# Optimization experiments

Measured on AMD Instinct MI355X. Metric: run time of the kernel, lower is better.

## Reference

```python
import jax, jax.numpy as jnp
import numpy as np

N = 2097152  # batch of 3x3 matrices


def setup_inputs() -> dict:
    key = jax.random.key(0)
    k1, k2 = jax.random.split(key)
    rotation = jax.random.normal(k1, (N, 3, 3), dtype=jnp.float32)
    # learned parameter: eye(3) + 1e-3 * randn, per __init__
    mat = jnp.eye(3, dtype=jnp.float32) + 0.001 * jax.random.normal(k2, (3, 3), dtype=jnp.float32)
    return {"rotation": rotation, "mat": mat}


def reference(rotation, mat):
    # new_mat = mat @ rotation (mat broadcast over batch)  -> [N,3,3]
    new_mat = jnp.einsum('ab,nbc->nac', mat, rotation)
    # polar rotation factor via batched 3x3 SVD: R = U @ V^T
    U, S, Vh = jnp.linalg.svd(new_mat, full_matrices=False)
    out = jnp.einsum('nab,nbc->nac', U, Vh)  # torch: U @ V.transpose == U @ Vh
    logdet = jnp.zeros((rotation.shape[0],), dtype=rotation.dtype)
    return out, logdet
```

## Files before the change

### kernel.cpp

```cpp
#include <hip/hip_runtime.h>
#include <math.h>


typedef float v2f __attribute__((ext_vector_type(2)));
typedef float v4f __attribute__((ext_vector_type(4)));

#define NEWTON_ITERS 6
#define NS_ITERS 2

__device__ __forceinline__ void polar_pair(
    v2f& x00, v2f& x01, v2f& x02,
    v2f& x10, v2f& x11, v2f& x12,
    v2f& x20, v2f& x21, v2f& x22)
{
    #pragma unroll
    for (int it = 0; it < NEWTON_ITERS; ++it) {
        v2f c00 = x11*x22 - x12*x21;
        v2f c01 = x12*x20 - x10*x22;
        v2f c02 = x10*x21 - x11*x20;
        v2f c10 = x02*x21 - x01*x22;
        v2f c11 = x00*x22 - x02*x20;
        v2f c12 = x01*x20 - x00*x21;
        v2f c20 = x01*x12 - x02*x11;
        v2f c21 = x02*x10 - x00*x12;
        v2f c22 = x00*x11 - x01*x10;

        v2f det = x00*c00 + x01*c01 + x02*c02;

        float d0 = det.x, d1 = det.y;
        float ad0 = fmaxf(fabsf(d0), 1e-30f);
        float ad1 = fmaxf(fabsf(d1), 1e-30f);
        float z0 = __builtin_amdgcn_exp2f(__builtin_amdgcn_logf(ad0) * (-1.0f/3.0f));
        float z1 = __builtin_amdgcn_exp2f(__builtin_amdgcn_logf(ad1) * (-1.0f/3.0f));
        v2f s = {0.5f * z0, 0.5f * z1};
        v2f u = {copysignf(0.5f * z0 * z0, d0), copysignf(0.5f * z1 * z1, d1)};

        x00 = s*x00 + u*c00;  x01 = s*x01 + u*c01;  x02 = s*x02 + u*c02;
        x10 = s*x10 + u*c10;  x11 = s*x11 + u*c11;  x12 = s*x12 + u*c12;
        x20 = s*x20 + u*c20;  x21 = s*x21 + u*c21;  x22 = s*x22 + u*c22;
    }

    #pragma unroll
    for (int it = 0; it < NS_ITERS; ++it) {
        v2f s00 = x00*x00 + x10*x10 + x20*x20;
        v2f s01 = x00*x01 + x10*x11 + x20*x21;
        v2f s02 = x00*x02 + x10*x12 + x20*x22;
        v2f s11 = x01*x01 + x11*x11 + x21*x21;
        v2f s12 = x01*x02 + x11*x12 + x21*x22;
        v2f s22 = x02*x02 + x12*x12 + x22*x22;
        v2f t00 = 1.5f - 0.5f*s00, t01 = -0.5f*s01, t02 = -0.5f*s02;
        v2f t11 = 1.5f - 0.5f*s11, t12 = -0.5f*s12;
        v2f t22 = 1.5f - 0.5f*s22;
        v2f y00 = x00*t00 + x01*t01 + x02*t02;
        v2f y01 = x00*t01 + x01*t11 + x02*t12;
        v2f y02 = x00*t02 + x01*t12 + x02*t22;
        v2f y10 = x10*t00 + x11*t01 + x12*t02;
        v2f y11 = x10*t01 + x11*t11 + x12*t12;
        v2f y12 = x10*t02 + x11*t12 + x12*t22;
        v2f y20 = x20*t00 + x21*t01 + x22*t02;
        v2f y21 = x20*t01 + x21*t11 + x22*t12;
        v2f y22 = x20*t02 + x21*t12 + x22*t22;
        x00=y00; x01=y01; x02=y02;
        x10=y10; x11=y11; x12=y12;
        x20=y20; x21=y21; x22=y22;
    }
}

__global__ __launch_bounds__(256) void polar3x3_wave_kernel(
    const float* __restrict__ rot,
    const float* __restrict__ mat,
    float* __restrict__ out,
    int n)
{
    __shared__ float lds[4608];
    const int t    = threadIdx.x;
    const int lane = t & 63;
    const int w    = t >> 6;
    const long long blockBase = (long long)blockIdx.x * 512;
    const long long waveBase  = blockBase + (long long)w * 128;
    float* wlds = lds + w * 1152;

    const float m00 = mat[0], m01 = mat[1], m02 = mat[2];
    const float m10 = mat[3], m11 = mat[4], m12 = mat[5];
    const float m20 = mat[6], m21 = mat[7], m22 = mat[8];

    const bool full = (blockBase + 512 <= (long long)n);

    v2f r00, r01, r02, r10, r11, r12, r20, r21, r22;

    if (full) {
        const float* gsrc = rot + waveBase * 9;
        #pragma unroll
        for (int k = 0; k < 4; ++k) {
            __builtin_amdgcn_global_load_lds(
                (const __attribute__((address_space(1))) void*)(gsrc + k * 256 + lane * 4),
                (__attribute__((address_space(3))) void*)(wlds + k * 256),
                16, 0, 0);
        }
        #pragma unroll
        for (int k = 0; k < 2; ++k) {
            __builtin_amdgcn_global_load_lds(
                (const __attribute__((address_space(1))) void*)(gsrc + 1024 + k * 64 + lane),
                (__attribute__((address_space(3))) void*)(wlds + 1024 + k * 64),
                4, 0, 0);
        }
        asm volatile("s_waitcnt vmcnt(0)" ::: "memory");

        const float* L = wlds + lane * 18;
        r00 = v2f{L[0], L[9]};  r01 = v2f{L[1], L[10]}; r02 = v2f{L[2], L[11]};
        r10 = v2f{L[3], L[12]}; r11 = v2f{L[4], L[13]}; r12 = v2f{L[5], L[14]};
        r20 = v2f{L[6], L[15]}; r21 = v2f{L[7], L[16]}; r22 = v2f{L[8], L[17]};
    } else {
        #pragma unroll
        for (int q = 0; q < 2; ++q) {
            long long mi = waveBase + 2 * lane + q;
            if (mi < (long long)n) {
                const float* r = rot + mi * 9;
                r00[q]=r[0]; r01[q]=r[1]; r02[q]=r[2];
                r10[q]=r[3]; r11[q]=r[4]; r12[q]=r[5];
                r20[q]=r[6]; r21[q]=r[7]; r22[q]=r[8];
            } else {
                r00[q]=1.f; r01[q]=0.f; r02[q]=0.f;
                r10[q]=0.f; r11[q]=1.f; r12[q]=0.f;
                r20[q]=0.f; r21[q]=0.f; r22[q]=1.f;
            }
        }
    }

    v2f x00 = m00*r00 + m01*r10 + m02*r20;
    v2f x01 = m00*r01 + m01*r11 + m02*r21;
    v2f x02 = m00*r02 + m01*r12 + m02*r22;
    v2f x10 = m10*r00 + m11*r10 + m12*r20;
    v2f x11 = m10*r01 + m11*r11 + m12*r21;
    v2f x12 = m10*r02 + m11*r12 + m12*r22;
    v2f x20 = m20*r00 + m21*r10 + m22*r20;
    v2f x21 = m20*r01 + m21*r11 + m22*r21;
    v2f x22 = m20*r02 + m21*r12 + m22*r22;

    polar_pair(x00,x01,x02,x10,x11,x12,x20,x21,x22);

    if (full) {
        float* S = wlds + lane * 18;
        S[0]=x00.x; S[9]=x00.y;  S[1]=x01.x; S[10]=x01.y;  S[2]=x02.x; S[11]=x02.y;
        S[3]=x10.x; S[12]=x10.y; S[4]=x11.x; S[13]=x11.y;  S[5]=x12.x; S[14]=x12.y;
        S[6]=x20.x; S[15]=x20.y; S[7]=x21.x; S[16]=x21.y;  S[8]=x22.x; S[17]=x22.y;
        v4f* gdst4 = (v4f*)(out + waveBase * 9);
        const v4f* l4 = (const v4f*)wlds;
        #pragma unroll
        for (int k = 0; k < 4; ++k)
            __builtin_nontemporal_store(l4[k * 64 + lane], gdst4 + k * 64 + lane);
        v2f* gdst2 = (v2f*)(out + waveBase * 9 + 1024);
        const v2f* l2 = (const v2f*)(wlds + 1024);
        __builtin_nontemporal_store(l2[lane], gdst2 + lane);

        v2f* ld2 = (v2f*)(out + (long long)n * 9 + waveBase);
        __builtin_nontemporal_store(v2f{0.f, 0.f}, ld2 + lane);
    } else {
        #pragma unroll
        for (int q = 0; q < 2; ++q) {
            long long mi = waveBase + 2 * lane + q;
            if (mi < (long long)n) {
                float* o = out + mi * 9;
                o[0]=x00[q]; o[1]=x01[q]; o[2]=x02[q];
                o[3]=x10[q]; o[4]=x11[q]; o[5]=x12[q];
                o[6]=x20[q]; o[7]=x21[q]; o[8]=x22[q];
                out[(long long)n * 9 + mi] = 0.0f;
            }
        }
    }
}

extern "C" void kernel_launch(void* const* d_in, const int* in_sizes, int n_in,
                              void* d_out, int out_size, void* d_ws, size_t ws_size,
                              hipStream_t stream) {
    const float* rot = (const float*)d_in[0];
    const float* mat = (const float*)d_in[1];
    float* out = (float*)d_out;

    int n = in_sizes[0] / 9;
    int block = 256;
    int grid = (n + 511) / 512;
    polar3x3_wave_kernel<<<grid, block, 0, stream>>>(rot, mat, out, n);
}
```

Baseline: 29.70 us.

## Process four matrices per thread with 128-thread blocks and wider LDS staging

Each thread now handles two pairs (four matrices) instead of one pair, with 128-thread blocks still covering 512 matrices. Global-to-LDS loads become nine 16-byte chunks per wave instead of mixed 16/4-byte loads, and the logdet zero-store is issued early so it overlaps the input loads. Output stores switch from nontemporal to regular stores. This adds instruction-level parallelism per thread but halves the thread count and raises register pressure, which may lower occupancy and latency hiding.

Result: slower. 32.27 us (+8.6%).

```diff
diff --git a/kernel.cpp b/kernel.cpp
--- a/kernel.cpp
+++ b/kernel.cpp
@@ -66,19 +66,30 @@
     }
 }
 
-__global__ __launch_bounds__(256) void polar3x3_wave_kernel(
+#define MATMUL_INIT(x, r)                                                     \
+    x##00 = m00*r##00 + m01*r##10 + m02*r##20;                                \
+    x##01 = m00*r##01 + m01*r##11 + m02*r##21;                                \
+    x##02 = m00*r##02 + m01*r##12 + m02*r##22;                                \
+    x##10 = m10*r##00 + m11*r##10 + m12*r##20;                                \
+    x##11 = m10*r##01 + m11*r##11 + m12*r##21;                                \
+    x##12 = m10*r##02 + m11*r##12 + m12*r##22;                                \
+    x##20 = m20*r##00 + m21*r##10 + m22*r##20;                                \
+    x##21 = m20*r##01 + m21*r##11 + m22*r##21;                                \
+    x##22 = m20*r##02 + m21*r##12 + m22*r##22;
+
+__global__ __launch_bounds__(128) void polar3x3_x4_kernel(
     const float* __restrict__ rot,
     const float* __restrict__ mat,
     float* __restrict__ out,
     int n)
 {
-    __shared__ float lds[4608];
+    __shared__ __align__(16) float lds[4608];
     const int t    = threadIdx.x;
     const int lane = t & 63;
     const int w    = t >> 6;
     const long long blockBase = (long long)blockIdx.x * 512;
-    const long long waveBase  = blockBase + (long long)w * 128;
-    float* wlds = lds + w * 1152;
+    const long long waveBase  = blockBase + (long long)w * 256;
+    float* wlds = lds + w * 2304;
 
     const float m00 = mat[0], m01 = mat[1], m02 = mat[2];
     const float m10 = mat[3], m11 = mat[4], m12 = mat[5];
@@ -86,85 +97,101 @@
 
     const bool full = (blockBase + 512 <= (long long)n);
 
-    v2f r00, r01, r02, r10, r11, r12, r20, r21, r22;
+    v2f a00,a01,a02,a10,a11,a12,a20,a21,a22;
+    v2f b00,b01,b02,b10,b11,b12,b20,b21,b22;
 
     if (full) {
         const float* gsrc = rot + waveBase * 9;
         #pragma unroll
-        for (int k = 0; k < 4; ++k) {
+        for (int k = 0; k < 9; ++k) {
             __builtin_amdgcn_global_load_lds(
                 (const __attribute__((address_space(1))) void*)(gsrc + k * 256 + lane * 4),
                 (__attribute__((address_space(3))) void*)(wlds + k * 256),
                 16, 0, 0);
         }
-        #pragma unroll
-        for (int k = 0; k < 2; ++k) {
-            __builtin_amdgcn_global_load_lds(
-                (const __attribute__((address_space(1))) void*)(gsrc + 1024 + k * 64 + lane),
-                (__attribute__((address_space(3))) void*)(wlds + 1024 + k * 64),
-                4, 0, 0);
+
+        v4f* ld4 = (v4f*)(out + (long long)n * 9 + waveBase);
+        __builtin_nontemporal_store(v4f{0.f, 0.f, 0.f, 0.f}, ld4 + lane);
+
+        asm volatile("s_waitcnt vmcnt(0)" ::: "memory");
+
+        const float* LA = wlds + lane * 18;
+        const float* LB = wlds + 1152 + lane * 18;
+        a00 = v2f{LA[0], LA[9]};  a01 = v2f{LA[1], LA[10]}; a02 = v2f{LA[2], LA[11]};
+        a10 = v2f{LA[3], LA[12]}; a11 = v2f{LA[4], LA[13]}; a12 = v2f{LA[5], LA[14]};
+        a20 = v2f{LA[6], LA[15]}; a21 = v2f{LA[7], LA[16]}; a22 = v2f{LA[8], LA[17]};
+        b00 = v2f{LB[0], LB[9]};  b01 = v2f{LB[1], LB[10]}; b02 = v2f{LB[2], LB[11]};
+        b10 = v2f{LB[3], LB[12]}; b11 = v2f{LB[4], LB[13]}; b12 = v2f{LB[5], LB[14]};
+        b20 = v2f{LB[6], LB[15]}; b21 = v2f{LB[7], LB[16]}; b22 = v2f{LB[8], LB[17]};
+    } else {
+        #pragma unroll
+        for (int q = 0; q < 2; ++q) {
+            long long miA = waveBase + 2 * lane + q;
+            long long miB = waveBase + 128 + 2 * lane + q;
+            if (miA < (long long)n) {
+                const float* r = rot + miA * 9;
+                a00[q]=r[0]; a01[q]=r[1]; a02[q]=r[2];
+                a10[q]=r[3]; a11[q]=r[4]; a12[q]=r[5];
+                a20[q]=r[6]; a21[q]=r[7]; a22[q]=r[8];
+            } else {
+                a00[q]=1.f; a01[q]=0.f; a02[q]=0.f;
+                a10[q]=0.f; a11[q]=1.f; a12[q]=0.f;
+                a20[q]=0.f; a21[q]=0.f; a22[q]=1.f;
+            }
+            if (miB < (long long)n) {
+                const float* r = rot + miB * 9;
+                b00[q]=r[0]; b01[q]=r[1]; b02[q]=r[2];
+                b10[q]=r[3]; b11[q]=r[4]; b12[q]=r[5];
+                b20[q]=r[6]; b21[q]=r[7]; b22[q]=r[8];
+            } else {
+                b00[q]=1.f; b01[q]=0.f; b02[q]=0.f;
+                b10[q]=0.f; b11[q]=1.f; b12[q]=0.f;
+                b20[q]=0.f; b21[q]=0.f; b22[q]=1.f;
+            }
         }
-        asm volatile("s_waitcnt vmcnt(0)" ::: "memory");
-
-        const float* L = wlds + lane * 18;
-        r00 = v2f{L[0], L[9]};  r01 = v2f{L[1], L[10]}; r02 = v2f{L[2], L[11]};
-        r10 = v2f{L[3], L[12]}; r11 = v2f{L[4], L[13]}; r12 = v2f{L[5], L[14]};
-        r20 = v2f{L[6], L[15]}; r21 = v2f{L[7], L[16]}; r22 = v2f{L[8], L[17]};
-    } else {
-        #pragma unroll
-        for (int q = 0; q < 2; ++q) {
-            long long mi = waveBase + 2 * lane + q;
-            if (mi < (long long)n) {
-                const float* r = rot + mi * 9;
-                r00[q]=r[0]; r01[q]=r[1]; r02[q]=r[2];
-                r10[q]=r[3]; r11[q]=r[4]; r12[q]=r[5];
-                r20[q]=r[6]; r21[q]=r[7]; r22[q]=r[8];
-            } else {
-                r00[q]=1.f; r01[q]=0.f; r02[q]=0.f;
-                r10[q]=0.f; r11[q]=1.f; r12[q]=0.f;
-                r20[q]=0.f; r21[q]=0.f; r22[q]=1.f;
-            }
-        }
-    }
-
-    v2f x00 = m00*r00 + m01*r10 + m02*r20;
-    v2f x01 = m00*r01 + m01*r11 + m02*r21;
-    v2f x02 = m00*r02 + m01*r12 + m02*r22;
-    v2f x10 = m10*r00 + m11*r10 + m12*r20;
-    v2f x11 = m10*r01 + m11*r11 + m12*r21;
-    v2f x12 = m10*r02 + m11*r12 + m12*r22;
-    v2f x20 = m20*r00 + m21*r10 + m22*r20;
-    v2f x21 = m20*r01 + m21*r11 + m22*r21;
-    v2f x22 = m20*r02 + m21*r12 + m22*r22;
-
-    polar_pair(x00,x01,x02,x10,x11,x12,x20,x21,x22);
+    }
+
+    v2f xa00,xa01,xa02,xa10,xa11,xa12,xa20,xa21,xa22;
+    v2f xb00,xb01,xb02,xb10,xb11,xb12,xb20,xb21,xb22;
+    MATMUL_INIT(xa, a)
+    MATMUL_INIT(xb, b)
+
+    polar_pair(xa00,xa01,xa02,xa10,xa11,xa12,xa20,xa21,xa22);
+    polar_pair(xb00,xb01,xb02,xb10,xb11,xb12,xb20,xb21,xb22);
 
     if (full) {
-        float* S = wlds + lane * 18;
-        S[0]=x00.x; S[9]=x00.y;  S[1]=x01.x; S[10]=x01.y;  S[2]=x02.x; S[11]=x02.y;
-        S[3]=x10.x; S[12]=x10.y; S[4]=x11.x; S[13]=x11.y;  S[5]=x12.x; S[14]=x12.y;
-        S[6]=x20.x; S[15]=x20.y; S[7]=x21.x; S[16]=x21.y;  S[8]=x22.x; S[17]=x22.y;
+        float* SA = wlds + lane * 18;
+        float* SB = wlds + 1152 + lane * 18;
+        SA[0]=xa00.x; SA[9] =xa00.y; SA[1]=xa01.x; SA[10]=xa01.y; SA[2]=xa02.x; SA[11]=xa02.y;
+        SA[3]=xa10.x; SA[12]=xa10.y; SA[4]=xa11.x; SA[13]=xa11.y; SA[5]=xa12.x; SA[14]=xa12.y;
+        SA[6]=xa20.x; SA[15]=xa20.y; SA[7]=xa21.x; SA[16]=xa21.y; SA[8]=xa22.x; SA[17]=xa22.y;
+        SB[0]=xb00.x; SB[9] =xb00.y; SB[1]=xb01.x; SB[10]=xb01.y; SB[2]=xb02.x; SB[11]=xb02.y;
+        SB[3]=xb10.x; SB[12]=xb10.y; SB[4]=xb11.x; SB[13]=xb11.y; SB[5]=xb12.x; SB[14]=xb12.y;
+        SB[6]=xb20.x; SB[15]=xb20.y; SB[7]=xb21.x; SB[16]=xb21.y; SB[8]=xb22.x; SB[17]=xb22.y;
+
         v4f* gdst4 = (v4f*)(out + waveBase * 9);
         const v4f* l4 = (const v4f*)wlds;
         #pragma unroll
-        for (int k = 0; k < 4; ++k)
-            __builtin_nontemporal_store(l4[k * 64 + lane], gdst4 + k * 64 + lane);
-        v2f* gdst2 = (v2f*)(out + waveBase * 9 + 1024);
-        const v2f* l2 = (const v2f*)(wlds + 1024);
-        __builtin_nontemporal_store(l2[lane], gdst2 + lane);
-
-        v2f* ld2 = (v2f*)(out + (long long)n * 9 + waveBase);
-        __builtin_nontemporal_store(v2f{0.f, 0.f}, ld2 + lane);
+        for (int k = 0; k < 9; ++k)
+            gdst4[k * 64 + lane] = l4[k * 64 + lane];
     } else {
         #pragma unroll
         for (int q = 0; q < 2; ++q) {
-            long long mi = waveBase + 2 * lane + q;
-            if (mi < (long long)n) {
-                float* o = out + mi * 9;
-                o[0]=x00[q]; o[1]=x01[q]; o[2]=x02[q];
-                o[3]=x10[q]; o[4]=x11[q]; o[5]=x12[q];
-                o[6]=x20[q]; o[7]=x21[q]; o[8]=x22[q];
-                out[(long long)n * 9 + mi] = 0.0f;
+            long long miA = waveBase + 2 * lane + q;
+            long long miB = waveBase + 128 + 2 * lane + q;
+            if (miA < (long long)n) {
+                float* o = out + miA * 9;
+                o[0]=xa00[q]; o[1]=xa01[q]; o[2]=xa02[q];
+                o[3]=xa10[q]; o[4]=xa11[q]; o[5]=xa12[q];
+                o[6]=xa20[q]; o[7]=xa21[q]; o[8]=xa22[q];
+                out[(long long)n * 9 + miA] = 0.0f;
+            }
+            if (miB < (long long)n) {
+                float* o = out + miB * 9;
+                o[0]=xb00[q]; o[1]=xb01[q]; o[2]=xb02[q];
+                o[3]=xb10[q]; o[4]=xb11[q]; o[5]=xb12[q];
+                o[6]=xb20[q]; o[7]=xb21[q]; o[8]=xb22[q];
+                out[(long long)n * 9 + miB] = 0.0f;
             }
         }
     }
@@ -178,7 +205,7 @@
     float* out = (float*)d_out;
 
     int n = in_sizes[0] / 9;
-    int block = 256;
+    int block = 128;
     int grid = (n + 511) / 512;
-    polar3x3_wave_kernel<<<grid, block, 0, stream>>>(rot, mat, out, n);
+    polar3x3_x4_kernel<<<grid, block, 0, stream>>>(rot, mat, out, n);
 }
```

## Double-buffer two tiles per wave to overlap second tile load with compute

Applied to the files above, without the earlier changes.

Each wave now handles two 128-matrix tiles with separate LDS buffers. It issues both tiles' global-to-LDS loads up front, then uses partial vmcnt waits so the second tile's load overlaps the first tile's polar iterations. The grid halves and LDS per block doubles, which can lower occupancy. Output stores switch from nontemporal to regular stores, and the logdet zeros go out as v4f.

Result: slower. 30.61 us (+3.0%).

```diff
diff --git a/kernel.cpp b/kernel.cpp
--- a/kernel.cpp
+++ b/kernel.cpp
@@ -66,66 +66,16 @@
     }
 }
 
-__global__ __launch_bounds__(256) void polar3x3_wave_kernel(
-    const float* __restrict__ rot,
-    const float* __restrict__ mat,
-    float* __restrict__ out,
-    int n)
-{
-    __shared__ float lds[4608];
-    const int t    = threadIdx.x;
-    const int lane = t & 63;
-    const int w    = t >> 6;
-    const long long blockBase = (long long)blockIdx.x * 512;
-    const long long waveBase  = blockBase + (long long)w * 128;
-    float* wlds = lds + w * 1152;
-
-    const float m00 = mat[0], m01 = mat[1], m02 = mat[2];
-    const float m10 = mat[3], m11 = mat[4], m12 = mat[5];
-    const float m20 = mat[6], m21 = mat[7], m22 = mat[8];
-
-    const bool full = (blockBase + 512 <= (long long)n);
-
-    v2f r00, r01, r02, r10, r11, r12, r20, r21, r22;
-
-    if (full) {
-        const float* gsrc = rot + waveBase * 9;
-        #pragma unroll
-        for (int k = 0; k < 4; ++k) {
-            __builtin_amdgcn_global_load_lds(
-                (const __attribute__((address_space(1))) void*)(gsrc + k * 256 + lane * 4),
-                (__attribute__((address_space(3))) void*)(wlds + k * 256),
-                16, 0, 0);
-        }
-        #pragma unroll
-        for (int k = 0; k < 2; ++k) {
-            __builtin_amdgcn_global_load_lds(
-                (const __attribute__((address_space(1))) void*)(gsrc + 1024 + k * 64 + lane),
-                (__attribute__((address_space(3))) void*)(wlds + 1024 + k * 64),
-                4, 0, 0);
-        }
-        asm volatile("s_waitcnt vmcnt(0)" ::: "memory");
-
-        const float* L = wlds + lane * 18;
-        r00 = v2f{L[0], L[9]};  r01 = v2f{L[1], L[10]}; r02 = v2f{L[2], L[11]};
-        r10 = v2f{L[3], L[12]}; r11 = v2f{L[4], L[13]}; r12 = v2f{L[5], L[14]};
-        r20 = v2f{L[6], L[15]}; r21 = v2f{L[7], L[16]}; r22 = v2f{L[8], L[17]};
-    } else {
-        #pragma unroll
-        for (int q = 0; q < 2; ++q) {
-            long long mi = waveBase + 2 * lane + q;
-            if (mi < (long long)n) {
-                const float* r = rot + mi * 9;
-                r00[q]=r[0]; r01[q]=r[1]; r02[q]=r[2];
-                r10[q]=r[3]; r11[q]=r[4]; r12[q]=r[5];
-                r20[q]=r[6]; r21[q]=r[7]; r22[q]=r[8];
-            } else {
-                r00[q]=1.f; r01[q]=0.f; r02[q]=0.f;
-                r10[q]=0.f; r11[q]=1.f; r12[q]=0.f;
-                r20[q]=0.f; r21[q]=0.f; r22[q]=1.f;
-            }
-        }
-    }
+__device__ __forceinline__ void compute_tile(
+    float* buf, int lane, float* outBase,
+    float m00, float m01, float m02,
+    float m10, float m11, float m12,
+    float m20, float m21, float m22)
+{
+    const float* L = buf + lane * 18;
+    v2f r00 = {L[0], L[9]},  r01 = {L[1], L[10]}, r02 = {L[2], L[11]};
+    v2f r10 = {L[3], L[12]}, r11 = {L[4], L[13]}, r12 = {L[5], L[14]};
+    v2f r20 = {L[6], L[15]}, r21 = {L[7], L[16]}, r22 = {L[8], L[17]};
 
     v2f x00 = m00*r00 + m01*r10 + m02*r20;
     v2f x01 = m00*r01 + m01*r11 + m02*r21;
@@ -139,32 +89,113 @@
 
     polar_pair(x00,x01,x02,x10,x11,x12,x20,x21,x22);
 
+    float* S = buf + lane * 18;
+    S[0]=x00.x; S[9] =x00.y; S[1]=x01.x; S[10]=x01.y; S[2]=x02.x; S[11]=x02.y;
+    S[3]=x10.x; S[12]=x10.y; S[4]=x11.x; S[13]=x11.y; S[5]=x12.x; S[14]=x12.y;
+    S[6]=x20.x; S[15]=x20.y; S[7]=x21.x; S[16]=x21.y; S[8]=x22.x; S[17]=x22.y;
+
+    v4f* g4 = (v4f*)outBase;
+    const v4f* l4 = (const v4f*)buf;
+    #pragma unroll
+    for (int k = 0; k < 4; ++k)
+        g4[k * 64 + lane] = l4[k * 64 + lane];
+    ((v2f*)(outBase + 1024))[lane] = ((const v2f*)(buf + 1024))[lane];
+}
+
+__device__ __forceinline__ void stage_tile(const float* gsrc, float* buf, int lane)
+{
+    #pragma unroll
+    for (int k = 0; k < 4; ++k) {
+        __builtin_amdgcn_global_load_lds(
+            (const __attribute__((address_space(1))) void*)(gsrc + k * 256 + lane * 4),
+            (__attribute__((address_space(3))) void*)(buf + k * 256),
+            16, 0, 0);
+    }
+    #pragma unroll
+    for (int k = 0; k < 2; ++k) {
+        __builtin_amdgcn_global_load_lds(
+            (const __attribute__((address_space(1))) void*)(gsrc + 1024 + k * 64 + lane),
+            (__attribute__((address_space(3))) void*)(buf + 1024 + k * 64),
+            4, 0, 0);
+    }
+}
+
+__global__ __launch_bounds__(256) void polar3x3_pipe_kernel(
+    const float* __restrict__ rot,
+    const float* __restrict__ mat,
+    float* __restrict__ out,
+    int n)
+{
+    __shared__ __align__(16) float lds[9216];
+    const int t    = threadIdx.x;
+    const int lane = t & 63;
+    const int w    = t >> 6;
+    const long long blockBase = (long long)blockIdx.x * 1024;
+    const long long waveBase  = blockBase + (long long)w * 256;
+    float* buf0 = lds + w * 2304;
+    float* buf1 = buf0 + 1152;
+
+    const float m00 = mat[0], m01 = mat[1], m02 = mat[2];
+    const float m10 = mat[3], m11 = mat[4], m12 = mat[5];
+    const float m20 = mat[6], m21 = mat[7], m22 = mat[8];
+
+    const bool full = (blockBase + 1024 <= (long long)n);
+
     if (full) {
-        float* S = wlds + lane * 18;
-        S[0]=x00.x; S[9]=x00.y;  S[1]=x01.x; S[10]=x01.y;  S[2]=x02.x; S[11]=x02.y;
-        S[3]=x10.x; S[12]=x10.y; S[4]=x11.x; S[13]=x11.y;  S[5]=x12.x; S[14]=x12.y;
-        S[6]=x20.x; S[15]=x20.y; S[7]=x21.x; S[16]=x21.y;  S[8]=x22.x; S[17]=x22.y;
-        v4f* gdst4 = (v4f*)(out + waveBase * 9);
-        const v4f* l4 = (const v4f*)wlds;
-        #pragma unroll
-        for (int k = 0; k < 4; ++k)
-            __builtin_nontemporal_store(l4[k * 64 + lane], gdst4 + k * 64 + lane);
-        v2f* gdst2 = (v2f*)(out + waveBase * 9 + 1024);
-        const v2f* l2 = (const v2f*)(wlds + 1024);
-        __builtin_nontemporal_store(l2[lane], gdst2 + lane);
-
-        v2f* ld2 = (v2f*)(out + (long long)n * 9 + waveBase);
-        __builtin_nontemporal_store(v2f{0.f, 0.f}, ld2 + lane);
+        stage_tile(rot + waveBase * 9, buf0, lane);
+        stage_tile(rot + (waveBase + 128) * 9, buf1, lane);
+
+        asm volatile("s_waitcnt vmcnt(6)" ::: "memory");
+
+        v4f* ld4 = (v4f*)(out + (long long)n * 9 + waveBase);
+        __builtin_nontemporal_store(v4f{0.f, 0.f, 0.f, 0.f}, ld4 + lane);
+
+        compute_tile(buf0, lane, out + waveBase * 9,
+                     m00,m01,m02,m10,m11,m12,m20,m21,m22);
+
+        asm volatile("s_waitcnt vmcnt(6)" ::: "memory");
+
+        compute_tile(buf1, lane, out + (waveBase + 128) * 9,
+                     m00,m01,m02,m10,m11,m12,m20,m21,m22);
     } else {
         #pragma unroll
-        for (int q = 0; q < 2; ++q) {
-            long long mi = waveBase + 2 * lane + q;
-            if (mi < (long long)n) {
-                float* o = out + mi * 9;
-                o[0]=x00[q]; o[1]=x01[q]; o[2]=x02[q];
-                o[3]=x10[q]; o[4]=x11[q]; o[5]=x12[q];
-                o[6]=x20[q]; o[7]=x21[q]; o[8]=x22[q];
-                out[(long long)n * 9 + mi] = 0.0f;
+        for (int tile = 0; tile < 2; ++tile) {
+            long long tileBase = waveBase + tile * 128;
+            v2f r00,r01,r02,r10,r11,r12,r20,r21,r22;
+            #pragma unroll
+            for (int q = 0; q < 2; ++q) {
+                long long mi = tileBase + 2 * lane + q;
+                if (mi < (long long)n) {
+                    const float* r = rot + mi * 9;
+                    r00[q]=r[0]; r01[q]=r[1]; r02[q]=r[2];
+                    r10[q]=r[3]; r11[q]=r[4]; r12[q]=r[5];
+                    r20[q]=r[6]; r21[q]=r[7]; r22[q]=r[8];
+                } else {
+                    r00[q]=1.f; r01[q]=0.f; r02[q]=0.f;
+                    r10[q]=0.f; r11[q]=1.f; r12[q]=0.f;
+                    r20[q]=0.f; r21[q]=0.f; r22[q]=1.f;
+                }
+            }
+            v2f x00 = m00*r00 + m01*r10 + m02*r20;
+            v2f x01 = m00*r01 + m01*r11 + m02*r21;
+            v2f x02 = m00*r02 + m01*r12 + m02*r22;
+            v2f x10 = m10*r00 + m11*r10 + m12*r20;
+            v2f x11 = m10*r01 + m11*r11 + m12*r21;
+            v2f x12 = m10*r02 + m11*r12 + m12*r22;
+            v2f x20 = m20*r00 + m21*r10 + m22*r20;
+            v2f x21 = m20*r01 + m21*r11 + m22*r21;
+            v2f x22 = m20*r02 + m21*r12 + m22*r22;
+            polar_pair(x00,x01,x02,x10,x11,x12,x20,x21,x22);
+            #pragma unroll
+            for (int q = 0; q < 2; ++q) {
+                long long mi = tileBase + 2 * lane + q;
+                if (mi < (long long)n) {
+                    float* o = out + mi * 9;
+                    o[0]=x00[q]; o[1]=x01[q]; o[2]=x02[q];
+                    o[3]=x10[q]; o[4]=x11[q]; o[5]=x12[q];
+                    o[6]=x20[q]; o[7]=x21[q]; o[8]=x22[q];
+                    out[(long long)n * 9 + mi] = 0.0f;
+                }
             }
         }
     }
@@ -179,6 +210,6 @@
 
     int n = in_sizes[0] / 9;
     int block = 256;
-    int grid = (n + 511) / 512;
-    polar3x3_wave_kernel<<<grid, block, 0, stream>>>(rot, mat, out, n);
-}
+    int grid = (n + 1023) / 1024;
+    polar3x3_pipe_kernel<<<grid, block, 0, stream>>>(rot, mat, out, n);
+}
```
